# Performance work log

Measured on AMD Instinct MI355X. Metric: run time of the kernel, lower is better.

## Reference

```python
import jax, jax.numpy as jnp
import numpy as np

B, IN, H, K, OUT = 2048, 512, 512, 32, 512


def setup_inputs() -> dict:
    key = jax.random.key(0)
    ks = jax.random.split(key, 14)
    s = 0.02
    return {
        "sample": jax.random.normal(ks[0], (B, IN), jnp.float32),
        "hidden": jax.random.normal(ks[1], (B, H), jnp.float32),
        "cell_tensor": jax.random.normal(ks[2], (K, B, H), jnp.float32),
        "d_0": jax.random.uniform(ks[3], (B, H), jnp.float32),
        "Wc": jax.random.normal(ks[4], (H, IN + H), jnp.float32) * s,
        "bc": jnp.zeros((H,), jnp.float32),
        "Wi": jax.random.normal(ks[5], (H, IN + H), jnp.float32) * s,
        "bi": jnp.zeros((H,), jnp.float32),
        "Wf": jax.random.normal(ks[6], (H, IN + 2 * H), jnp.float32) * s,
        "bf": jnp.zeros((H,), jnp.float32),
        "Wo": jax.random.normal(ks[7], (H, IN + H), jnp.float32) * s,
        "bo": jnp.zeros((H,), jnp.float32),
        "Wout": jax.random.normal(ks[8], (OUT, H), jnp.float32) * s,
        "bout": jnp.zeros((OUT,), jnp.float32),
    }


def _fractional_weights(d, k):
    # Closed form of get_ws: w[j] = prod_{i=0}^{k-1-j} (i - d)/(i+1)
    # Vectorized over all (batch, hidden) elements at once.
    i = jnp.arange(k, dtype=d.dtype)[:, None, None]  # [k,1,1]
    factors = (i - d[None]) / (i + 1.0)              # [k,B,H]
    return jnp.flip(jnp.cumprod(factors, axis=0), axis=0)  # [k,B,H]


def reference(sample, hidden, cell_tensor, d_0, Wc, bc, Wi, bi, Wf, bf, Wo, bo, Wout, bout):
    k = cell_tensor.shape[0]
    combined = jnp.concatenate([sample, hidden], axis=1)            # [B, IN+H]
    combined_d = jnp.concatenate([sample, hidden, d_0], axis=1)     # [B, IN+2H]

    d_values = jax.nn.sigmoid(combined_d @ Wf.T + bf) * 0.5         # [B,H]

    w = _fractional_weights(d_values, k)                            # [k,B,H]
    first = -jnp.sum(cell_tensor * w, axis=0)                       # [B,H]

    i_gate = jax.nn.sigmoid(combined @ Wi.T + bi)
    o_gate = jax.nn.sigmoid(combined @ Wo.T + bo)
    c_tilde = jnp.tanh(combined @ Wc.T + bc)

    cell = first + c_tilde * i_gate                                 # [B,H]
    h_c_1 = jnp.concatenate([cell_tensor, cell[None]], axis=0)[1:]  # [k,B,H]
    hidden_new = jnp.tanh(cell) * o_gate                            # [B,H]
    output = hidden_new @ Wout.T + bout                             # [B,OUT]
    return (output, hidden_new, h_c_1, d_values)
```

## Files before the change

### kernel.cpp

```cpp
#include <hip/hip_runtime.h>
#include <hip/hip_bf16.h>
#include <math.h>

#define BB   2048
#define INH  512
#define HH   512
#define KK   32
#define OUTD 512
#define KDIM 1536
#define NG   2048

typedef __attribute__((ext_vector_type(8))) short short8;
typedef __attribute__((ext_vector_type(4))) float floatx4;

__device__ __forceinline__ void async_copy16(void* lds, const void* g) {
  __builtin_amdgcn_global_load_lds(
      (const __attribute__((address_space(1))) unsigned int*)g,
      (__attribute__((address_space(3))) unsigned int*)lds,
      16, 0, 0);
}

__device__ __forceinline__ float sigmoidf_(float x) {
  return 1.0f / (1.0f + __expf(-x));
}

__device__ __forceinline__ unsigned short to_bf16(float f) {
  __hip_bfloat16 h = __float2bfloat16(f);
  return *reinterpret_cast<unsigned short*>(&h);
}

__global__ __launch_bounds__(256) void pack_kernel(
    const float* __restrict__ sample, const float* __restrict__ hidden,
    const float* __restrict__ d0,
    const float* __restrict__ Wc, const float* __restrict__ Wi,
    const float* __restrict__ Wf, const float* __restrict__ Wo,
    const float* __restrict__ Wout,
    unsigned short* __restrict__ Abf, unsigned short* __restrict__ Wbf,
    unsigned short* __restrict__ Woutbf)
{
  const int NA = BB * KDIM;
  int i = blockIdx.x * 256 + threadIdx.x;
  if (i < NA) {
    int r = i / KDIM, c = i - r * KDIM;
    float v = (c < 512) ? sample[r * 512 + c]
            : (c < 1024) ? hidden[r * 512 + (c - 512)]
                         : d0[r * 512 + (c - 1024)];
    Abf[i] = to_bf16(v);
  } else if (i < 2 * NA) {
    int j = i - NA;
    int g = j / KDIM, c = j - g * KDIM;
    int q = g >> 9, h = g & 511;
    float v;
    if (q == 0)           v = Wf[(size_t)h * 1536 + c];
    else if (c >= 1024)   v = 0.0f;
    else if (q == 1)      v = Wi[(size_t)h * 1024 + c];
    else if (q == 2)      v = Wo[(size_t)h * 1024 + c];
    else                  v = Wc[(size_t)h * 1024 + c];
    Wbf[j] = to_bf16(v);
  } else {
    int j = i - 2 * NA;
    Woutbf[j] = to_bf16(Wout[j]);
  }
}

template<int MODE>
__global__ __launch_bounds__(256) void gemm_bf16(
    const unsigned short* __restrict__ A,
    const unsigned short* __restrict__ Bw,
    int M, int N, int K,
    const float* __restrict__ bias0, const float* __restrict__ bias1,
    const float* __restrict__ bias2, const float* __restrict__ bias3,
    float* __restrict__ o0, float* __restrict__ o1,
    float* __restrict__ o2, float* __restrict__ o3)
{
  __shared__ __align__(16) unsigned short As[128 * 32];
  __shared__ __align__(16) unsigned short Bs[128 * 32];
  const int tid  = threadIdx.x;
  const int lane = tid & 63;
  const int wid  = tid >> 6;
  const int wr   = wid >> 1, wc = wid & 1;
  const int tm   = blockIdx.y * 128, tn = blockIdx.x * 128;

  floatx4 acc[4][4];
  #pragma unroll
  for (int mi = 0; mi < 4; ++mi)
    #pragma unroll
    for (int ni = 0; ni < 4; ++ni)
      acc[mi][ni] = (floatx4){0.f, 0.f, 0.f, 0.f};

  for (int k0 = 0; k0 < K; k0 += 32) {
    #pragma unroll
    for (int p = 0; p < 2; ++p) {
      int c   = tid + p * 256;
      int row = c >> 2;
      int kg  = (c & 3) << 3;
      async_copy16(&As[c * 8], &A[(size_t)(tm + row) * K + k0 + kg]);
      async_copy16(&Bs[c * 8], &Bw[(size_t)(tn + row) * K + k0 + kg]);
    }
    asm volatile("s_waitcnt vmcnt(0)" ::: "memory");
    __syncthreads();

    short8 af[4], bf8[4];
    const int kb  = (lane >> 4) << 3;
    const int r16 = lane & 15;
    #pragma unroll
    for (int mi = 0; mi < 4; ++mi)
      af[mi] = *(const short8*)&As[(wr * 64 + mi * 16 + r16) * 32 + kb];
    #pragma unroll
    for (int ni = 0; ni < 4; ++ni)
      bf8[ni] = *(const short8*)&Bs[(wc * 64 + ni * 16 + r16) * 32 + kb];

    #pragma unroll
    for (int mi = 0; mi < 4; ++mi)
      #pragma unroll
      for (int ni = 0; ni < 4; ++ni)
        acc[mi][ni] = __builtin_amdgcn_mfma_f32_16x16x32_bf16(
            af[mi], bf8[ni], acc[mi][ni], 0, 0, 0);
    __syncthreads();
  }

  #pragma unroll
  for (int mi = 0; mi < 4; ++mi) {
    const int row0 = tm + wr * 64 + mi * 16 + (lane >> 4) * 4;
    #pragma unroll
    for (int ni = 0; ni < 4; ++ni) {
      const int col = tn + wc * 64 + ni * 16 + (lane & 15);
      floatx4 v = acc[mi][ni];
      if (MODE == 0) {
        const int gate = col >> 9;
        const int h    = col & 511;
        #pragma unroll
        for (int r = 0; r < 4; ++r) {
          const int row = row0 + r;
          float x = v[r];
          if (gate == 0)      o0[(size_t)row * 512 + h] = 0.5f * sigmoidf_(x + bias0[h]);
          else if (gate == 1) o1[(size_t)row * 512 + h] = sigmoidf_(x + bias1[h]);
          else if (gate == 2) o2[(size_t)row * 512 + h] = sigmoidf_(x + bias2[h]);
          else                o3[(size_t)row * 512 + h] = tanhf(x + bias3[h]);
        }
      } else {
        #pragma unroll
        for (int r = 0; r < 4; ++r) {
          const int row = row0 + r;
          o0[(size_t)row * N + col] = v[r] + bias0[col];
        }
      }
    }
  }
}

__global__ __launch_bounds__(256) void cell_kernel(
    const float4* __restrict__ ct,
    const float4* __restrict__ dv,
    const float4* __restrict__ ig,
    const float4* __restrict__ og,
    const float4* __restrict__ cg,
    float4* __restrict__ hc1,
    float4* __restrict__ hnew,
    ushort4* __restrict__ hbf)
{
  const int NBH4 = (BB * HH) / 4;
  const int idx  = blockIdx.x * 256 + threadIdx.x;

  float4 d = dv[idx];
  float px = 1.f, py = 1.f, pz = 1.f, pw = 1.f;
  float fx = 0.f, fy = 0.f, fz = 0.f, fw = 0.f;

  #pragma unroll
  for (int i = 0; i < 32; ++i) {
    const int j = 31 - i;
    float4 c = ct[(size_t)j * NBH4 + idx];
    const float inv = 1.0f / (float)(i + 1);
    const float fi  = (float)i;
    px *= (fi - d.x) * inv;  py *= (fi - d.y) * inv;
    pz *= (fi - d.z) * inv;  pw *= (fi - d.w) * inv;
    fx -= c.x * px;  fy -= c.y * py;
    fz -= c.z * pz;  fw -= c.w * pw;
    if (j >= 1) hc1[(size_t)(j - 1) * NBH4 + idx] = c;
  }

  float4 iv = ig[idx], ov = og[idx], cv = cg[idx];
  float4 cell;
  cell.x = fx + cv.x * iv.x;  cell.y = fy + cv.y * iv.y;
  cell.z = fz + cv.z * iv.z;  cell.w = fw + cv.w * iv.w;
  hc1[(size_t)31 * NBH4 + idx] = cell;

  float4 hn;
  hn.x = tanhf(cell.x) * ov.x;  hn.y = tanhf(cell.y) * ov.y;
  hn.z = tanhf(cell.z) * ov.z;  hn.w = tanhf(cell.w) * ov.w;
  hnew[idx] = hn;

  ushort4 hb;
  hb.x = to_bf16(hn.x);  hb.y = to_bf16(hn.y);
  hb.z = to_bf16(hn.z);  hb.w = to_bf16(hn.w);
  hbf[idx] = hb;
}

extern "C" void kernel_launch(void* const* d_in, const int* in_sizes, int n_in,
                              void* d_out, int out_size, void* d_ws, size_t ws_size,
                              hipStream_t stream) {
  const float* sample = (const float*)d_in[0];
  const float* hidden = (const float*)d_in[1];
  const float* cell_t = (const float*)d_in[2];
  const float* d0     = (const float*)d_in[3];
  const float* Wc     = (const float*)d_in[4];
  const float* bc     = (const float*)d_in[5];
  const float* Wi     = (const float*)d_in[6];
  const float* bi     = (const float*)d_in[7];
  const float* Wf     = (const float*)d_in[8];
  const float* bf     = (const float*)d_in[9];
  const float* Wo     = (const float*)d_in[10];
  const float* bo     = (const float*)d_in[11];
  const float* Wout   = (const float*)d_in[12];
  const float* bout   = (const float*)d_in[13];

  float* out        = (float*)d_out;
  float* out_hidden = out + (size_t)BB * OUTD;
  float* out_hc1    = out_hidden + (size_t)BB * HH;
  float* out_dv     = out_hc1 + (size_t)KK * BB * HH;

  char* ws = (char*)d_ws;
  unsigned short* Abf    = (unsigned short*)ws;
  unsigned short* Wbf    = Abf + (size_t)BB * KDIM;
  unsigned short* Woutbf = Wbf + (size_t)NG * KDIM;
  float* ig  = (float*)(Woutbf + (size_t)OUTD * HH);
  float* og  = ig + (size_t)BB * HH;
  float* cg  = og + (size_t)BB * HH;
  unsigned short* hbf = (unsigned short*)(cg + (size_t)BB * HH);

  pack_kernel<<<25600, 256, 0, stream>>>(sample, hidden, d0, Wc, Wi, Wf, Wo,
                                         Wout, Abf, Wbf, Woutbf);
  gemm_bf16<0><<<dim3(16, 16), 256, 0, stream>>>(
      Abf, Wbf, BB, NG, KDIM, bf, bi, bo, bc, out_dv, ig, og, cg);
  cell_kernel<<<1024, 256, 0, stream>>>(
      (const float4*)cell_t, (const float4*)out_dv, (const float4*)ig,
      (const float4*)og, (const float4*)cg, (float4*)out_hc1,
      (float4*)out_hidden, (ushort4*)hbf);
  gemm_bf16<1><<<dim3(4, 16), 256, 0, stream>>>(
      hbf, Woutbf, BB, OUTD, HH, bout, nullptr, nullptr, nullptr,
      out, nullptr, nullptr, nullptr);
}
```

Measured before the change: 363.1 us.

## Double-buffer GEMM K-tiles with XOR-swizzled LDS layout and vectorized packing

Measured after the change: 332.4 us. -8.5%, faster.

```diff
diff --git a/kernel.cpp b/kernel.cpp
--- a/kernel.cpp
+++ b/kernel.cpp
@@ -3,7 +3,6 @@
 #include <math.h>
 
 #define BB   2048
-#define INH  512
 #define HH   512
 #define KK   32
 #define OUTD 512
@@ -29,7 +28,8 @@
   return *reinterpret_cast<unsigned short*>(&h);
 }
 
-__global__ __launch_bounds__(256) void pack_kernel(
+
+__global__ __launch_bounds__(192) void pack_kernel(
     const float* __restrict__ sample, const float* __restrict__ hidden,
     const float* __restrict__ d0,
     const float* __restrict__ Wc, const float* __restrict__ Wi,
@@ -38,112 +38,179 @@
     unsigned short* __restrict__ Abf, unsigned short* __restrict__ Wbf,
     unsigned short* __restrict__ Woutbf)
 {
-  const int NA = BB * KDIM;
-  int i = blockIdx.x * 256 + threadIdx.x;
-  if (i < NA) {
-    int r = i / KDIM, c = i - r * KDIM;
-    float v = (c < 512) ? sample[r * 512 + c]
-            : (c < 1024) ? hidden[r * 512 + (c - 512)]
-                         : d0[r * 512 + (c - 1024)];
-    Abf[i] = to_bf16(v);
-  } else if (i < 2 * NA) {
-    int j = i - NA;
-    int g = j / KDIM, c = j - g * KDIM;
-    int q = g >> 9, h = g & 511;
-    float v;
-    if (q == 0)           v = Wf[(size_t)h * 1536 + c];
-    else if (c >= 1024)   v = 0.0f;
-    else if (q == 1)      v = Wi[(size_t)h * 1024 + c];
-    else if (q == 2)      v = Wo[(size_t)h * 1024 + c];
-    else                  v = Wc[(size_t)h * 1024 + c];
-    Wbf[j] = to_bf16(v);
+  const int r  = blockIdx.x;
+  const int qq = threadIdx.x;
+  float4 v0, v1;
+
+  if (r < 2048) {
+    const int k0 = qq * 8;
+    const float* src = (k0 < 512)  ? sample + (size_t)r * 512 + k0
+                     : (k0 < 1024) ? hidden + (size_t)r * 512 + (k0 - 512)
+                                   : d0     + (size_t)r * 512 + (k0 - 1024);
+    v0 = ((const float4*)src)[0];
+    v1 = ((const float4*)src)[1];
+    const int dc = (qq & ~7) | ((qq & 7) ^ (r & 7));
+    short8 o;
+    o[0]=to_bf16(v0.x); o[1]=to_bf16(v0.y); o[2]=to_bf16(v0.z); o[3]=to_bf16(v0.w);
+    o[4]=to_bf16(v1.x); o[5]=to_bf16(v1.y); o[6]=to_bf16(v1.z); o[7]=to_bf16(v1.w);
+    *(short8*)&Abf[(size_t)r * KDIM + dc * 8] = o;
+  } else if (r < 4096) {
+    const int g = r - 2048;
+    const int q4 = g >> 9, h = g & 511;
+    const int k0 = qq * 8;
+    if (q4 == 0) {
+      const float* s = Wf + (size_t)h * 1536 + k0;
+      v0 = ((const float4*)s)[0]; v1 = ((const float4*)s)[1];
+    } else if (k0 >= 1024) {
+      v0 = make_float4(0.f,0.f,0.f,0.f); v1 = v0;
+    } else {
+      const float* s = (q4 == 1 ? Wi : q4 == 2 ? Wo : Wc) + (size_t)h * 1024 + k0;
+      v0 = ((const float4*)s)[0]; v1 = ((const float4*)s)[1];
+    }
+    const int dc = (qq & ~7) | ((qq & 7) ^ (g & 7));
+    short8 o;
+    o[0]=to_bf16(v0.x); o[1]=to_bf16(v0.y); o[2]=to_bf16(v0.z); o[3]=to_bf16(v0.w);
+    o[4]=to_bf16(v1.x); o[5]=to_bf16(v1.y); o[6]=to_bf16(v1.z); o[7]=to_bf16(v1.w);
+    *(short8*)&Wbf[(size_t)g * KDIM + dc * 8] = o;
   } else {
-    int j = i - 2 * NA;
-    Woutbf[j] = to_bf16(Wout[j]);
+    const int rw = r - 4096;
+    if (qq < 64) {
+      const int k0 = qq * 8;
+      const float* s = Wout + (size_t)rw * 512 + k0;
+      v0 = ((const float4*)s)[0]; v1 = ((const float4*)s)[1];
+      const int dc = (qq & ~7) | ((qq & 7) ^ (rw & 7));
+      short8 o;
+      o[0]=to_bf16(v0.x); o[1]=to_bf16(v0.y); o[2]=to_bf16(v0.z); o[3]=to_bf16(v0.w);
+      o[4]=to_bf16(v1.x); o[5]=to_bf16(v1.y); o[6]=to_bf16(v1.z); o[7]=to_bf16(v1.w);
+      *(short8*)&Woutbf[(size_t)rw * 512 + dc * 8] = o;
+    }
   }
 }
 
-template<int MODE>
-__global__ __launch_bounds__(256) void gemm_bf16(
+template<int BM, int BN, int MODE>
+__global__ __launch_bounds__(256) void gemm2(
     const unsigned short* __restrict__ A,
     const unsigned short* __restrict__ Bw,
-    int M, int N, int K,
+    int K, int NT, int N,
     const float* __restrict__ bias0, const float* __restrict__ bias1,
     const float* __restrict__ bias2, const float* __restrict__ bias3,
     float* __restrict__ o0, float* __restrict__ o1,
     float* __restrict__ o2, float* __restrict__ o3)
 {
-  __shared__ __align__(16) unsigned short As[128 * 32];
-  __shared__ __align__(16) unsigned short Bs[128 * 32];
+  constexpr int MI = BM / 32, NI = BN / 32;
+  __shared__ __align__(16) unsigned short As[2][BM * 64];
+  __shared__ __align__(16) unsigned short Bs[2][BN * 64];
   const int tid  = threadIdx.x;
   const int lane = tid & 63;
   const int wid  = tid >> 6;
   const int wr   = wid >> 1, wc = wid & 1;
-  const int tm   = blockIdx.y * 128, tn = blockIdx.x * 128;
-
-  floatx4 acc[4][4];
+  const int tm   = blockIdx.y * BM, tn = blockIdx.x * BN;
+
+  floatx4 acc[MI][NI];
   #pragma unroll
-  for (int mi = 0; mi < 4; ++mi)
-    #pragma unroll
-    for (int ni = 0; ni < 4; ++ni)
+  for (int mi = 0; mi < MI; ++mi)
+    #pragma unroll
+    for (int ni = 0; ni < NI; ++ni)
       acc[mi][ni] = (floatx4){0.f, 0.f, 0.f, 0.f};
 
-  for (int k0 = 0; k0 < K; k0 += 32) {
-    #pragma unroll
-    for (int p = 0; p < 2; ++p) {
-      int c   = tid + p * 256;
-      int row = c >> 2;
-      int kg  = (c & 3) << 3;
-      async_copy16(&As[c * 8], &A[(size_t)(tm + row) * K + k0 + kg]);
-      async_copy16(&Bs[c * 8], &Bw[(size_t)(tn + row) * K + k0 + kg]);
-    }
-    asm volatile("s_waitcnt vmcnt(0)" ::: "memory");
+  const char* Abase = (const char*)A;
+  const char* Bbase = (const char*)Bw;
+  const size_t rowbytes = (size_t)K * 2;
+
+  auto stage = [&](int buf, int t) {
+    #pragma unroll
+    for (int p = 0; p < BM * 8 / 256; ++p) {
+      const int c = tid + p * 256;
+      const int row = c >> 3, ci = c & 7;
+      async_copy16(&As[buf][c * 8],
+                   Abase + (size_t)(tm + row) * rowbytes + (size_t)t * 128 + ci * 16);
+    }
+    #pragma unroll
+    for (int p = 0; p < BN * 8 / 256; ++p) {
+      const int c = tid + p * 256;
+      const int row = c >> 3, ci = c & 7;
+      async_copy16(&Bs[buf][c * 8],
+                   Bbase + (size_t)(tn + row) * rowbytes + (size_t)t * 128 + ci * 16);
+    }
+  };
+
+  stage(0, 0);
+  const int r16 = lane & 15, kq = lane >> 4;
+
+  for (int t = 0; t < NT; ++t) {
+    const int cur = t & 1;
+    if (t + 1 < NT) {
+      stage(cur ^ 1, t + 1);
+      if constexpr (BM + BN == 256)
+        asm volatile("s_waitcnt vmcnt(8)" ::: "memory");
+      else
+        asm volatile("s_waitcnt vmcnt(4)" ::: "memory");
+    } else {
+      asm volatile("s_waitcnt vmcnt(0)" ::: "memory");
+    }
     __syncthreads();
 
-    short8 af[4], bf8[4];
-    const int kb  = (lane >> 4) << 3;
-    const int r16 = lane & 15;
-    #pragma unroll
-    for (int mi = 0; mi < 4; ++mi)
-      af[mi] = *(const short8*)&As[(wr * 64 + mi * 16 + r16) * 32 + kb];
-    #pragma unroll
-    for (int ni = 0; ni < 4; ++ni)
-      bf8[ni] = *(const short8*)&Bs[(wc * 64 + ni * 16 + r16) * 32 + kb];
-
-    #pragma unroll
-    for (int mi = 0; mi < 4; ++mi)
-      #pragma unroll
-      for (int ni = 0; ni < 4; ++ni)
-        acc[mi][ni] = __builtin_amdgcn_mfma_f32_16x16x32_bf16(
-            af[mi], bf8[ni], acc[mi][ni], 0, 0, 0);
+    #pragma unroll
+    for (int ks = 0; ks < 2; ++ks) {
+      short8 af[MI], bfr[NI];
+      #pragma unroll
+      for (int mi = 0; mi < MI; ++mi) {
+        const int r  = wr * (BM / 2) + mi * 16 + r16;
+        const int pc = (ks * 4 + kq) ^ (r & 7);
+        af[mi] = *(const short8*)&As[cur][r * 64 + pc * 8];
+      }
+      #pragma unroll
+      for (int ni = 0; ni < NI; ++ni) {
+        const int r  = wc * (BN / 2) + ni * 16 + r16;
+        const int pc = (ks * 4 + kq) ^ (r & 7);
+        bfr[ni] = *(const short8*)&Bs[cur][r * 64 + pc * 8];
+      }
+      #pragma unroll
+      for (int mi = 0; mi < MI; ++mi)
+        #pragma unroll
+        for (int ni = 0; ni < NI; ++ni)
+          acc[mi][ni] = __builtin_amdgcn_mfma_f32_16x16x32_bf16(
+              af[mi], bfr[ni], acc[mi][ni], 0, 0, 0);
+    }
     __syncthreads();
   }
 
-  #pragma unroll
-  for (int mi = 0; mi < 4; ++mi) {
-    const int row0 = tm + wr * 64 + mi * 16 + (lane >> 4) * 4;
-    #pragma unroll
-    for (int ni = 0; ni < 4; ++ni) {
-      const int col = tn + wc * 64 + ni * 16 + (lane & 15);
-      floatx4 v = acc[mi][ni];
-      if (MODE == 0) {
-        const int gate = col >> 9;
-        const int h    = col & 511;
+  if (MODE == 0) {
+    const int gate = tn >> 9;
+    float* og   = (gate == 0) ? o0 : (gate == 1) ? o1 : (gate == 2) ? o2 : o3;
+    const float* bg = (gate == 0) ? bias0 : (gate == 1) ? bias1
+                    : (gate == 2) ? bias2 : bias3;
+    #pragma unroll
+    for (int mi = 0; mi < MI; ++mi) {
+      const int row0 = tm + wr * (BM / 2) + mi * 16 + (lane >> 4) * 4;
+      #pragma unroll
+      for (int ni = 0; ni < NI; ++ni) {
+        const int col = tn + wc * (BN / 2) + ni * 16 + (lane & 15);
+        const int h   = col & 511;
+        const float b = bg[h];
+        floatx4 v = acc[mi][ni];
         #pragma unroll
         for (int r = 0; r < 4; ++r) {
-          const int row = row0 + r;
-          float x = v[r];
-          if (gate == 0)      o0[(size_t)row * 512 + h] = 0.5f * sigmoidf_(x + bias0[h]);
-          else if (gate == 1) o1[(size_t)row * 512 + h] = sigmoidf_(x + bias1[h]);
-          else if (gate == 2) o2[(size_t)row * 512 + h] = sigmoidf_(x + bias2[h]);
-          else                o3[(size_t)row * 512 + h] = tanhf(x + bias3[h]);
+          const float x = v[r] + b;
+          float res;
+          if (gate == 0)      res = 0.5f * sigmoidf_(x);
+          else if (gate == 3) res = tanhf(x);
+          else                res = sigmoidf_(x);
+          og[(size_t)(row0 + r) * 512 + h] = res;
         }
-      } else {
+      }
+    }
+  } else {
+    #pragma unroll
+    for (int mi = 0; mi < MI; ++mi) {
+      const int row0 = tm + wr * (BM / 2) + mi * 16 + (lane >> 4) * 4;
+      #pragma unroll
+      for (int ni = 0; ni < NI; ++ni) {
+        const int col = tn + wc * (BN / 2) + ni * 16 + (lane & 15);
+        floatx4 v = acc[mi][ni];
         #pragma unroll
-        for (int r = 0; r < 4; ++r) {
-          const int row = row0 + r;
-          o0[(size_t)row * N + col] = v[r] + bias0[col];
-        }
+        for (int r = 0; r < 4; ++r)
+          o0[(size_t)(row0 + r) * N + col] = v[r] + bias0[col];
       }
     }
   }
@@ -157,29 +224,37 @@
     const float4* __restrict__ cg,
     float4* __restrict__ hc1,
     float4* __restrict__ hnew,
-    ushort4* __restrict__ hbf)
+    unsigned short* __restrict__ hbf)
 {
   const int NBH4 = (BB * HH) / 4;
   const int idx  = blockIdx.x * 256 + threadIdx.x;
 
-  float4 d = dv[idx];
+  const float4 d = dv[idx];
   float px = 1.f, py = 1.f, pz = 1.f, pw = 1.f;
   float fx = 0.f, fy = 0.f, fz = 0.f, fw = 0.f;
 
   #pragma unroll
-  for (int i = 0; i < 32; ++i) {
-    const int j = 31 - i;
-    float4 c = ct[(size_t)j * NBH4 + idx];
-    const float inv = 1.0f / (float)(i + 1);
-    const float fi  = (float)i;
-    px *= (fi - d.x) * inv;  py *= (fi - d.y) * inv;
-    pz *= (fi - d.z) * inv;  pw *= (fi - d.w) * inv;
-    fx -= c.x * px;  fy -= c.y * py;
-    fz -= c.z * pz;  fw -= c.w * pw;
-    if (j >= 1) hc1[(size_t)(j - 1) * NBH4 + idx] = c;
+  for (int g = 7; g >= 0; --g) {
+    float4 c3 = ct[(size_t)(4 * g + 3) * NBH4 + idx];
+    float4 c2 = ct[(size_t)(4 * g + 2) * NBH4 + idx];
+    float4 c1 = ct[(size_t)(4 * g + 1) * NBH4 + idx];
+    float4 c0 = ct[(size_t)(4 * g + 0) * NBH4 + idx];
+    #pragma unroll
+    for (int s = 3; s >= 0; --s) {
+      const int j = 4 * g + s;
+      const int i = 31 - j;
+      const float inv = 1.0f / (float)(i + 1);
+      const float fi  = (float)i;
+      const float4 c = (s == 3) ? c3 : (s == 2) ? c2 : (s == 1) ? c1 : c0;
+      px *= (fi - d.x) * inv;  py *= (fi - d.y) * inv;
+      pz *= (fi - d.z) * inv;  pw *= (fi - d.w) * inv;
+      fx -= c.x * px;  fy -= c.y * py;
+      fz -= c.z * pz;  fw -= c.w * pw;
+      if (j >= 1) hc1[(size_t)(j - 1) * NBH4 + idx] = c;
+    }
   }
 
-  float4 iv = ig[idx], ov = og[idx], cv = cg[idx];
+  const float4 iv = ig[idx], ov = og[idx], cv = cg[idx];
   float4 cell;
   cell.x = fx + cv.x * iv.x;  cell.y = fy + cv.y * iv.y;
   cell.z = fz + cv.z * iv.z;  cell.w = fw + cv.w * iv.w;
@@ -190,10 +265,14 @@
   hn.z = tanhf(cell.z) * ov.z;  hn.w = tanhf(cell.w) * ov.w;
   hnew[idx] = hn;
 
+  const int b  = idx >> 7;
+  const int h0 = (idx & 127) * 4;
+  const int qc = h0 >> 3;
+  const int dc = (qc & ~7) | ((qc & 7) ^ (b & 7));
   ushort4 hb;
   hb.x = to_bf16(hn.x);  hb.y = to_bf16(hn.y);
   hb.z = to_bf16(hn.z);  hb.w = to_bf16(hn.w);
-  hbf[idx] = hb;
+  *(ushort4*)&hbf[(size_t)b * 512 + dc * 8 + (h0 & 7)] = hb;
 }
 
 extern "C" void kernel_launch(void* const* d_in, const int* in_sizes, int n_in,
@@ -228,15 +307,15 @@
   float* cg  = og + (size_t)BB * HH;
   unsigned short* hbf = (unsigned short*)(cg + (size_t)BB * HH);
 
-  pack_kernel<<<25600, 256, 0, stream>>>(sample, hidden, d0, Wc, Wi, Wf, Wo,
-                                         Wout, Abf, Wbf, Woutbf);
-  gemm_bf16<0><<<dim3(16, 16), 256, 0, stream>>>(
-      Abf, Wbf, BB, NG, KDIM, bf, bi, bo, bc, out_dv, ig, og, cg);
+  pack_kernel<<<4608, 192, 0, stream>>>(sample, hidden, d0, Wc, Wi, Wf, Wo,
+                                        Wout, Abf, Wbf, Woutbf);
+  gemm2<128, 128, 0><<<dim3(16, 16), 256, 0, stream>>>(
+      Abf, Wbf, KDIM, KDIM / 64, NG, bf, bi, bo, bc, out_dv, ig, og, cg);
   cell_kernel<<<1024, 256, 0, stream>>>(
       (const float4*)cell_t, (const float4*)out_dv, (const float4*)ig,
       (const float4*)og, (const float4*)cg, (float4*)out_hc1,
-      (float4*)out_hidden, (ushort4*)hbf);
-  gemm_bf16<1><<<dim3(4, 16), 256, 0, stream>>>(
-      hbf, Woutbf, BB, OUTD, HH, bout, nullptr, nullptr, nullptr,
+      (float4*)out_hidden, hbf);
+  gemm2<64, 64, 1><<<dim3(8, 32), 256, 0, stream>>>(
+      hbf, Woutbf, HH, HH / 64, OUTD, bout, nullptr, nullptr, nullptr,
       out, nullptr, nullptr, nullptr);
 }
```
